# Kernel tuning notes

Hardware: AMD Instinct MI355X
Metric: run time of the kernel (lower is better)

## Reference

```python
import jax, jax.numpy as jnp
import numpy as np

D_MODEL = 1024
NUM_HEADS = 16
HEAD_DIM = D_MODEL // NUM_HEADS
THETA = 10000.0


def setup_inputs() -> dict:
    key = jax.random.key(0)
    k1, k2, k3 = jax.random.split(key, 3)
    B, S = 4, 2048
    std_qkv = (2.0 / (D_MODEL + 3 * D_MODEL)) ** 0.5
    std_out = (2.0 / (D_MODEL + D_MODEL)) ** 0.5
    return {
        "x": jax.random.normal(k1, (B, S, D_MODEL), dtype=jnp.float32),
        "token_positions": jnp.arange(S, dtype=jnp.int64 if jax.config.jax_enable_x64 else jnp.int32),
        "w_qkv": jax.random.normal(k2, (3 * D_MODEL, D_MODEL), dtype=jnp.float32) * std_qkv,
        "w_out": jax.random.normal(k3, (D_MODEL, D_MODEL), dtype=jnp.float32) * std_out,
    }


def _apply_rope(x, token_positions):
    # x: [b, h, s, d_h]; token_positions: [s]
    inv_freq = 1.0 / (THETA ** (jnp.arange(0, HEAD_DIM, 2, dtype=jnp.float32) / HEAD_DIM))
    angles = token_positions.astype(jnp.float32)[:, None] * inv_freq  # [s, d_h/2]
    cos, sin = jnp.cos(angles), jnp.sin(angles)
    x_even = x[..., 0::2]
    x_odd = x[..., 1::2]
    out_even = x_even * cos - x_odd * sin
    out_odd = x_even * sin + x_odd * cos
    # re-interleave even/odd lanes
    return jnp.stack([out_even, out_odd], axis=-1).reshape(x.shape)


def reference(x, token_positions, w_qkv, w_out):
    B, S, _ = x.shape
    qkv = jnp.einsum("bsd,ed->bse", x, w_qkv)  # [b, s, 3*d_model]
    q, k, v = jnp.split(qkv, 3, axis=-1)

    def to_heads(t):  # [b, s, d_model] -> [b, h, s, d_h]
        return t.reshape(B, S, NUM_HEADS, HEAD_DIM).transpose(0, 2, 1, 3)

    q, k, v = to_heads(q), to_heads(k), to_heads(v)
    q = _apply_rope(q, token_positions)
    k = _apply_rope(k, token_positions)

    scale = 1.0 / (HEAD_DIM ** 0.5)
    scores = jnp.einsum("bhqd,bhkd->bhqk", q, k) * scale  # [b, h, s, s]
    causal = jnp.tril(jnp.ones((S, S), dtype=bool))
    scores = jnp.where(causal, scores, -jnp.inf)
    probs = jax.nn.softmax(scores, axis=-1)
    out = jnp.einsum("bhqk,bhkd->bhqd", probs, v)  # [b, h, s, d_h]
    out = out.transpose(0, 2, 1, 3).reshape(B, S, D_MODEL)
    return jnp.einsum("bsd,ed->bse", out, w_out)
```

## Files before the change

### kernel.cpp

```cpp
#include <hip/hip_runtime.h>

typedef unsigned short u16;
typedef __attribute__((ext_vector_type(4))) float f32x4;
typedef __attribute__((ext_vector_type(8))) __bf16 bf16x8;
typedef __attribute__((ext_vector_type(8))) short short8;
typedef __attribute__((ext_vector_type(4))) u16 u16x4;

__device__ __forceinline__ u16 f2bf(float f) {
    union { float f; unsigned u; } v; v.f = f;
    unsigned r = v.u + 0x7fffu + ((v.u >> 16) & 1u);
    return (u16)(r >> 16);
}

__device__ __forceinline__ f32x4 mfma16(bf16x8 a, bf16x8 b, f32x4 c) {
    return __builtin_amdgcn_mfma_f32_16x16x32_bf16(a, b, c, 0, 0, 0);
}

__device__ __forceinline__ void gload16(const u16* g, u16* lds) {
    __builtin_amdgcn_global_load_lds(
        (const __attribute__((address_space(1))) void*)g,
        (__attribute__((address_space(3))) void*)lds, 16, 0, 0);
}

__global__ void cvt_bf16_kernel(const float* __restrict__ src, u16* __restrict__ dst, int n4) {
    int i = blockIdx.x * blockDim.x + threadIdx.x;
    if (i >= n4) return;
    float4 v = ((const float4*)src)[i];
    u16x4 o = { f2bf(v.x), f2bf(v.y), f2bf(v.z), f2bf(v.w) };
    *(u16x4*)&dst[i * 4] = o;
}

__global__ void rope_tbl_kernel(const int* __restrict__ pos, float2* __restrict__ tbl) {
    int i = blockIdx.x * blockDim.x + threadIdx.x;
    int s = i >> 5, p = i & 31;
    float inv = powf(10000.0f, -(float)p / 32.0f);
    float a = (float)pos[s] * inv;
    float sn, cs;
    sincosf(a, &sn, &cs);
    tbl[i] = make_float2(cs, sn);
}

template<int MODE>
__global__ __launch_bounds__(256) void gemm_bt(
    const u16* __restrict__ A, const u16* __restrict__ B,
    float* __restrict__ C, int N,
    u16* __restrict__ Qt, u16* __restrict__ Ktn, u16* __restrict__ VTt,
    const float2* __restrict__ tbl)
{
    __shared__ alignas(16) u16 As[128 * 32];
    __shared__ alignas(16) u16 Bs[128 * 32];
    const int t = threadIdx.x;
    const int l = t & 63, w = t >> 6;
    const int lg = l >> 4, lc = l & 15;
    const int wr = w >> 1, wc = w & 1;
    const int brow = blockIdx.y * 128, bcol = blockIdx.x * 128;
    const int sr = w * 16 + (l >> 2), sc = (l & 3) * 8;
    const u16* ga = A + (size_t)(brow + sr) * 1024 + sc;
    const u16* gb = B + (size_t)(bcol + sr) * 1024 + sc;
    u16* la = &As[w * 512];
    u16* lb = &Bs[w * 512];
    f32x4 acc[4][4] = {};

    for (int kt = 0; kt < 1024; kt += 32) {
        __syncthreads();
        gload16(ga + kt, la);
        gload16(ga + 64 * 1024 + kt, la + 2048);
        gload16(gb + kt, lb);
        gload16(gb + 64 * 1024 + kt, lb + 2048);
        __syncthreads();
        bf16x8 af[4], bfr[4];
#pragma unroll
        for (int i = 0; i < 4; ++i)
            af[i] = *(const bf16x8*)&As[(wr * 64 + i * 16 + lc) * 32 + lg * 8];
#pragma unroll
        for (int j = 0; j < 4; ++j)
            bfr[j] = *(const bf16x8*)&Bs[(wc * 64 + j * 16 + lc) * 32 + lg * 8];
#pragma unroll
        for (int i = 0; i < 4; ++i)
#pragma unroll
            for (int j = 0; j < 4; ++j)
                acc[i][j] = mfma16(af[i], bfr[j], acc[i][j]);
    }

    if (MODE == 0) {
#pragma unroll
        for (int i = 0; i < 4; ++i) {
            int row = brow + wr * 64 + i * 16 + lg * 4;
#pragma unroll
            for (int j = 0; j < 4; ++j) {
                int col = bcol + wc * 64 + j * 16 + lc;
#pragma unroll
                for (int jj = 0; jj < 4; ++jj)
                    C[(size_t)(row + jj) * N + col] = acc[i][j][jj];
            }
        }
    } else {
        const int b = brow >> 11;
#pragma unroll
        for (int i = 0; i < 4; ++i) {
            int s0 = (brow & 2047) + wr * 64 + i * 16 + lg * 4;
#pragma unroll
            for (int j = 0; j < 4; ++j) {
                int e0 = bcol + wc * 64 + j * 16;
                int region = e0 >> 10;
                int er = e0 & 1023;
                int h = er >> 6;
                int d = (er & 63) + lc;
                size_t bh = (size_t)(b * 16 + h);
                if (region <= 1) {
                    int p = d >> 1;
                    float sgn = (d & 1) ? 1.0f : -1.0f;
                    u16* dst = (region == 0) ? Qt : Ktn;
                    float mul = (region == 0) ? 0.18033688011112043f : 1.0f;
#pragma unroll
                    for (int jj = 0; jj < 4; ++jj) {
                        float v = acc[i][j][jj];
                        float pr = __shfl_xor(v, 1);
                        float2 cs = tbl[(size_t)(s0 + jj) * 32 + p];
                        float o = (v * cs.x + pr * cs.y * sgn) * mul;
                        int s = s0 + jj;
                        int dd = (region == 0) ? d : (d ^ ((s & 7) << 3));
                        dst[((size_t)bh * 2048 + s) * 64 + dd] = f2bf(o);
                    }
                } else {
                    int tile = s0 >> 6, r = s0 & 63;
                    int p0 = ((r >> 5) << 5) + (((r >> 2) & 3) << 3) + (((r >> 4) & 1) << 2);
                    int idx = (tile << 6) + (p0 ^ ((d & 7) << 3));
                    u16x4 pk;
#pragma unroll
                    for (int jj = 0; jj < 4; ++jj) pk[jj] = f2bf(acc[i][j][jj]);
                    *(u16x4*)&VTt[((size_t)bh * 64 + d) * 2048 + idx] = pk;
                }
            }
        }
    }
}

__global__ __launch_bounds__(256, 4) void attn_kernel(
    const u16* __restrict__ Qt, const u16* __restrict__ Kswz,
    const u16* __restrict__ Vp, u16* __restrict__ O)
{
    __shared__ alignas(16) u16 Kl[2][64 * 64];
    __shared__ alignas(16) u16 Vl[2][64 * 64];
    const int bid = blockIdx.x;
    const int qt = 15 - (bid >> 6);
    const int bh = bid & 63;
    const int t = threadIdx.x, l = t & 63, w = t >> 6;
    const int lg = l >> 4, lc = l & 15;
    const int qb0 = qt * 128 + w * 32;
    const int ntiles = 2 * qt + 2;
    const int swz = (lc & 7) << 3;

    bf16x8 qf[2][2];
#pragma unroll
    for (int f = 0; f < 2; ++f)
#pragma unroll
        for (int fk = 0; fk < 2; ++fk)
            qf[f][fk] = *(const bf16x8*)&Qt[((size_t)bh * 2048 + qb0 + 16 * f + lc) * 64 + fk * 32 + lg * 8];

    const bf16x8 ones = { (__bf16)1.f, (__bf16)1.f, (__bf16)1.f, (__bf16)1.f,
                          (__bf16)1.f, (__bf16)1.f, (__bf16)1.f, (__bf16)1.f };

    f32x4 aco[2][4] = {};
    f32x4 aco_sum[2] = {};
    float m[2] = { -1e30f, -1e30f };

    const int srow = t >> 3;
    const int scol = (t & 7) * 8;
    const u16* gK = Kswz + (size_t)bh * 131072;
    const u16* gV = Vp + (size_t)bh * 131072;

    auto stage = [&](int buf, int kv0) {
        gload16(gK + ((size_t)(kv0 + srow) << 6) + scol,      &Kl[buf][srow * 64 + scol]);
        gload16(gK + ((size_t)(kv0 + srow + 32) << 6) + scol, &Kl[buf][(srow + 32) * 64 + scol]);
        gload16(gV + (size_t)srow * 2048 + kv0 + scol,        &Vl[buf][srow * 64 + scol]);
        gload16(gV + (size_t)(srow + 32) * 2048 + kv0 + scol, &Vl[buf][(srow + 32) * 64 + scol]);
    };

    stage(0, 0);
    __syncthreads();
    int cur = 0;

    for (int kt = 0; kt < ntiles; ++kt) {
        const int kv0 = kt * 64;
        if (kt + 1 < ntiles) stage(cur ^ 1, kv0 + 64);

        if (kv0 <= qb0 + 31) {
            const u16* Kc = Kl[cur];
            const u16* Vc = Vl[cur];

            f32x4 sc[2][4];
            const f32x4 zf = { 0.f, 0.f, 0.f, 0.f };
#pragma unroll
            for (int nb = 0; nb < 4; ++nb) {
                const u16* kr = &Kc[(nb * 16 + lc) * 64];
                bf16x8 kb0 = *(const bf16x8*)&kr[(lg * 8) ^ swz];
                bf16x8 kb1 = *(const bf16x8*)&kr[(32 + lg * 8) ^ swz];
                sc[0][nb] = mfma16(kb0, qf[0][0], zf);
                sc[0][nb] = mfma16(kb1, qf[0][1], sc[0][nb]);
                sc[1][nb] = mfma16(kb0, qf[1][0], zf);
                sc[1][nb] = mfma16(kb1, qf[1][1], sc[1][nb]);
            }

            float pm[2];
#pragma unroll
            for (int f = 0; f < 2; ++f) {
                if (kv0 + 63 > qb0 + 16 * f) {
                    const int qq = qb0 + 16 * f + lc;
#pragma unroll
                    for (int nb = 0; nb < 4; ++nb) {
                        const int kb = kv0 + nb * 16 + lg * 4;
#pragma unroll
                        for (int jj = 0; jj < 4; ++jj)
                            if (kb + jj > qq) sc[f][nb][jj] = -1e38f;
                    }
                }
                float a0 = fmaxf(fmaxf(sc[f][0][0], sc[f][0][1]), fmaxf(sc[f][0][2], sc[f][0][3]));
                float a1 = fmaxf(fmaxf(sc[f][1][0], sc[f][1][1]), fmaxf(sc[f][1][2], sc[f][1][3]));
                float a2 = fmaxf(fmaxf(sc[f][2][0], sc[f][2][1]), fmaxf(sc[f][2][2], sc[f][2][3]));
                float a3 = fmaxf(fmaxf(sc[f][3][0], sc[f][3][1]), fmaxf(sc[f][3][2], sc[f][3][3]));
                float a = fmaxf(fmaxf(a0, a1), fmaxf(a2, a3));
                a = fmaxf(a, __shfl_xor(a, 16));
                a = fmaxf(a, __shfl_xor(a, 32));
                pm[f] = a;
            }

            int need = (pm[0] > m[0] + 11.0f) || (pm[1] > m[1] + 11.0f);
            if (__any(need)) {
#pragma unroll
                for (int f = 0; f < 2; ++f) {
                    float mn = fmaxf(m[f], pm[f]);
                    float scal = exp2f(m[f] - mn);
                    m[f] = mn;
                    aco_sum[f][0] *= scal;
#pragma unroll
                    for (int nb = 0; nb < 4; ++nb) aco[f][nb] *= scal;
                }
            }

            bf16x8 pB[2][2];
#pragma unroll
            for (int f = 0; f < 2; ++f) {
#pragma unroll
                for (int nb = 0; nb < 4; ++nb)
#pragma unroll
                    for (int jj = 0; jj < 4; ++jj)
                        sc[f][nb][jj] = exp2f(sc[f][nb][jj] - m[f]);
#pragma unroll
                for (int fk = 0; fk < 2; ++fk) {
                    bf16x8 pb;
#pragma unroll
                    for (int e = 0; e < 4; ++e) {
                        pb[e]     = (__bf16)sc[f][2 * fk][e];
                        pb[e + 4] = (__bf16)sc[f][2 * fk + 1][e];
                    }
                    pB[f][fk] = pb;
                }
            }

#pragma unroll
            for (int nb = 0; nb < 4; ++nb) {
                const u16* vr = &Vc[(nb * 16 + lc) * 64];
#pragma unroll
                for (int fk = 0; fk < 2; ++fk) {
                    bf16x8 va = *(const bf16x8*)&vr[(fk * 32 + lg * 8) ^ swz];
                    aco[0][nb] = mfma16(va, pB[0][fk], aco[0][nb]);
                    aco[1][nb] = mfma16(va, pB[1][fk], aco[1][nb]);
                }
            }
#pragma unroll
            for (int f = 0; f < 2; ++f) {
                aco_sum[f] = mfma16(ones, pB[f][0], aco_sum[f]);
                aco_sum[f] = mfma16(ones, pB[f][1], aco_sum[f]);
            }
        }

        __syncthreads();
        cur ^= 1;
    }

    const int b = bh >> 4, h = bh & 15;
#pragma unroll
    for (int f = 0; f < 2; ++f) {
        float rinv = 1.0f / aco_sum[f][0];
        size_t row = (size_t)b * 2048 + qb0 + 16 * f + lc;
#pragma unroll
        for (int nb = 0; nb < 4; ++nb) {
            u16x4 pk;
#pragma unroll
            for (int jj = 0; jj < 4; ++jj) pk[jj] = f2bf(aco[f][nb][jj] * rinv);
            *(u16x4*)&O[row * 1024 + h * 64 + nb * 16 + lg * 4] = pk;
        }
    }
}

extern "C" void kernel_launch(void* const* d_in, const int* in_sizes, int n_in,
                              void* d_out, int out_size, void* d_ws, size_t ws_size,
                              hipStream_t stream) {
    const float* x    = (const float*)d_in[0];
    const int*   pos  = (const int*)d_in[1];
    const float* wqkv = (const float*)d_in[2];
    const float* wout = (const float*)d_in[3];
    float* out = (float*)d_out;
    char* ws = (char*)d_ws;

    u16*    x_bf    = (u16*)(ws);
    u16*    wqkv_bf = (u16*)(ws + 16777216);
    u16*    wout_bf = (u16*)(ws + 23068672);
    float2* tbl     = (float2*)(ws + 25165824);
    u16*    Qt      = (u16*)(ws + 25690112);
    u16*    Kt      = (u16*)(ws + 42467328);
    u16*    VTt     = (u16*)(ws + 59244544);
    u16*    O       = (u16*)(ws + 76021760);
    if (ws_size < 92798976u) return;

    cvt_bf16_kernel<<<8192, 256, 0, stream>>>(x, x_bf, 2097152);
    cvt_bf16_kernel<<<3072, 256, 0, stream>>>(wqkv, wqkv_bf, 786432);
    cvt_bf16_kernel<<<1024, 256, 0, stream>>>(wout, wout_bf, 262144);
    rope_tbl_kernel<<<256, 256, 0, stream>>>(pos, tbl);

    dim3 g1(24, 64);
    gemm_bt<1><<<g1, 256, 0, stream>>>(x_bf, wqkv_bf, nullptr, 0, Qt, Kt, VTt, tbl);

    attn_kernel<<<1024, 256, 0, stream>>>(Qt, Kt, VTt, O);

    dim3 g2(8, 64);
    gemm_bt<0><<<g2, 256, 0, stream>>>(O, wout_bf, out, 1024, nullptr, nullptr, nullptr, nullptr);
}
```

Baseline: 310.0 us.

## Load V fragments directly from global in MFMA order, stage 128-row K tiles

The QKV projection now writes V in a fragment-major layout, so each lane's bf16x8 MFMA operand is contiguous. The attention kernel reads V straight from global/L2 into registers instead of staging it through LDS, and stages K in 128-row tiles processed as two 64-row subtiles, which halves the number of barriers per block. It also reorders query-tile scheduling to interleave heavy and light causal tiles, and raises wave priority around the MFMA sections. The aim is to cut LDS traffic and synchronisation cost. In exchange, V loads now expose global-memory latency inside the loop, and the larger K buffer uses the same total LDS.

```diff
diff --git a/kernel.cpp b/kernel.cpp
--- a/kernel.cpp
+++ b/kernel.cpp
@@ -124,12 +124,14 @@
                     }
                 } else {
                     int tile = s0 >> 6, r = s0 & 63;
-                    int p0 = ((r >> 5) << 5) + (((r >> 2) & 3) << 3) + (((r >> 4) & 1) << 2);
-                    int idx = (tile << 6) + (p0 ^ ((d & 7) << 3));
+                    int fk = r >> 5, lgg = (r >> 2) & 3, eb = ((r >> 4) & 1) * 4;
+                    size_t off = bh * 131072 + (size_t)tile * 4096 +
+                                 (size_t)(d >> 4) * 1024 + fk * 512 + lgg * 128 +
+                                 (d & 15) * 8 + eb;
                     u16x4 pk;
 #pragma unroll
                     for (int jj = 0; jj < 4; ++jj) pk[jj] = f2bf(acc[i][j][jj]);
-                    *(u16x4*)&VTt[((size_t)bh * 64 + d) * 2048 + idx] = pk;
+                    *(u16x4*)&VTt[off] = pk;
                 }
             }
         }
@@ -138,17 +140,20 @@
 
 __global__ __launch_bounds__(256, 4) void attn_kernel(
     const u16* __restrict__ Qt, const u16* __restrict__ Kswz,
-    const u16* __restrict__ Vp, u16* __restrict__ O)
+    const u16* __restrict__ Vg, u16* __restrict__ O)
 {
-    __shared__ alignas(16) u16 Kl[2][64 * 64];
-    __shared__ alignas(16) u16 Vl[2][64 * 64];
+    __shared__ alignas(16) u16 Kl[2][128 * 64];
     const int bid = blockIdx.x;
-    const int qt = 15 - (bid >> 6);
+    const int rr_ = bid >> 8, aa_ = (bid >> 6) & 3;
     const int bh = bid & 63;
+    const int qt = (rr_ == 0) ? 15 - 2 * aa_
+                 : (rr_ == 1) ? 8 + 2 * aa_
+                 : (rr_ == 2) ? 7 - 2 * aa_
+                              : 2 * aa_;
     const int t = threadIdx.x, l = t & 63, w = t >> 6;
     const int lg = l >> 4, lc = l & 15;
     const int qb0 = qt * 128 + w * 32;
-    const int ntiles = 2 * qt + 2;
+    const int ntiles = qt + 1;
     const int swz = (lc & 7) << 3;
 
     bf16x8 qf[2][2];
@@ -168,110 +173,122 @@
     const int srow = t >> 3;
     const int scol = (t & 7) * 8;
     const u16* gK = Kswz + (size_t)bh * 131072;
-    const u16* gV = Vp + (size_t)bh * 131072;
-
-    auto stage = [&](int buf, int kv0) {
-        gload16(gK + ((size_t)(kv0 + srow) << 6) + scol,      &Kl[buf][srow * 64 + scol]);
-        gload16(gK + ((size_t)(kv0 + srow + 32) << 6) + scol, &Kl[buf][(srow + 32) * 64 + scol]);
-        gload16(gV + (size_t)srow * 2048 + kv0 + scol,        &Vl[buf][srow * 64 + scol]);
-        gload16(gV + (size_t)(srow + 32) * 2048 + kv0 + scol, &Vl[buf][(srow + 32) * 64 + scol]);
+    const u16* gV = Vg + (size_t)bh * 131072 + l * 8;
+
+    auto stageK = [&](int buf, int kv0) {
+#pragma unroll
+        for (int c = 0; c < 4; ++c)
+            gload16(gK + ((size_t)(kv0 + srow + 32 * c) << 6) + scol,
+                    &Kl[buf][(srow + 32 * c) * 64 + scol]);
     };
 
-    stage(0, 0);
+    stageK(0, 0);
     __syncthreads();
     int cur = 0;
 
     for (int kt = 0; kt < ntiles; ++kt) {
-        const int kv0 = kt * 64;
-        if (kt + 1 < ntiles) stage(cur ^ 1, kv0 + 64);
-
-        if (kv0 <= qb0 + 31) {
-            const u16* Kc = Kl[cur];
-            const u16* Vc = Vl[cur];
-
-            f32x4 sc[2][4];
-            const f32x4 zf = { 0.f, 0.f, 0.f, 0.f };
-#pragma unroll
-            for (int nb = 0; nb < 4; ++nb) {
-                const u16* kr = &Kc[(nb * 16 + lc) * 64];
-                bf16x8 kb0 = *(const bf16x8*)&kr[(lg * 8) ^ swz];
-                bf16x8 kb1 = *(const bf16x8*)&kr[(32 + lg * 8) ^ swz];
-                sc[0][nb] = mfma16(kb0, qf[0][0], zf);
-                sc[0][nb] = mfma16(kb1, qf[0][1], sc[0][nb]);
-                sc[1][nb] = mfma16(kb0, qf[1][0], zf);
-                sc[1][nb] = mfma16(kb1, qf[1][1], sc[1][nb]);
-            }
-
-            float pm[2];
-#pragma unroll
-            for (int f = 0; f < 2; ++f) {
-                if (kv0 + 63 > qb0 + 16 * f) {
-                    const int qq = qb0 + 16 * f + lc;
-#pragma unroll
-                    for (int nb = 0; nb < 4; ++nb) {
-                        const int kb = kv0 + nb * 16 + lg * 4;
+        const int kv0 = kt * 128;
+        if (kt + 1 < ntiles) stageK(cur ^ 1, kv0 + 128);
+
+#pragma unroll
+        for (int sub = 0; sub < 2; ++sub) {
+            const int kvs = kv0 + sub * 64;
+            if (kvs <= qb0 + 31) {
+                const u16* Kc = &Kl[cur][(sub << 6) * 64];
+
+                f32x4 sc[2][4];
+                const f32x4 zf = { 0.f, 0.f, 0.f, 0.f };
+                __builtin_amdgcn_s_setprio(1);
+#pragma unroll
+                for (int nb = 0; nb < 4; ++nb) {
+                    const u16* kr = &Kc[(nb * 16 + lc) * 64];
+                    bf16x8 kb0 = *(const bf16x8*)&kr[(lg * 8) ^ swz];
+                    bf16x8 kb1 = *(const bf16x8*)&kr[(32 + lg * 8) ^ swz];
+                    sc[0][nb] = mfma16(kb0, qf[0][0], zf);
+                    sc[0][nb] = mfma16(kb1, qf[0][1], sc[0][nb]);
+                    sc[1][nb] = mfma16(kb0, qf[1][0], zf);
+                    sc[1][nb] = mfma16(kb1, qf[1][1], sc[1][nb]);
+                }
+                __builtin_amdgcn_s_setprio(0);
+
+                float pm[2];
+#pragma unroll
+                for (int f = 0; f < 2; ++f) {
+                    if (kvs + 63 > qb0 + 16 * f) {
+                        const int qq = qb0 + 16 * f + lc;
+#pragma unroll
+                        for (int nb = 0; nb < 4; ++nb) {
+                            const int kb = kvs + nb * 16 + lg * 4;
+#pragma unroll
+                            for (int jj = 0; jj < 4; ++jj)
+                                if (kb + jj > qq) sc[f][nb][jj] = -1e38f;
+                        }
+                    }
+                    float a0 = fmaxf(fmaxf(sc[f][0][0], sc[f][0][1]), fmaxf(sc[f][0][2], sc[f][0][3]));
+                    float a1 = fmaxf(fmaxf(sc[f][1][0], sc[f][1][1]), fmaxf(sc[f][1][2], sc[f][1][3]));
+                    float a2 = fmaxf(fmaxf(sc[f][2][0], sc[f][2][1]), fmaxf(sc[f][2][2], sc[f][2][3]));
+                    float a3 = fmaxf(fmaxf(sc[f][3][0], sc[f][3][1]), fmaxf(sc[f][3][2], sc[f][3][3]));
+                    float a = fmaxf(fmaxf(a0, a1), fmaxf(a2, a3));
+                    a = fmaxf(a, __shfl_xor(a, 16));
+                    a = fmaxf(a, __shfl_xor(a, 32));
+                    pm[f] = a;
+                }
+
+                int need = (pm[0] > m[0] + 11.0f) || (pm[1] > m[1] + 11.0f);
+                if (__any(need)) {
+#pragma unroll
+                    for (int f = 0; f < 2; ++f) {
+                        float mn = fmaxf(m[f], pm[f]);
+                        float scal = exp2f(m[f] - mn);
+                        m[f] = mn;
+                        aco_sum[f][0] *= scal;
+#pragma unroll
+                        for (int nb = 0; nb < 4; ++nb) aco[f][nb] *= scal;
+                    }
+                }
+
+                bf16x8 pB[2][2];
+#pragma unroll
+                for (int f = 0; f < 2; ++f) {
+#pragma unroll
+                    for (int nb = 0; nb < 4; ++nb)
 #pragma unroll
                         for (int jj = 0; jj < 4; ++jj)
-                            if (kb + jj > qq) sc[f][nb][jj] = -1e38f;
-                    }
-                }
-                float a0 = fmaxf(fmaxf(sc[f][0][0], sc[f][0][1]), fmaxf(sc[f][0][2], sc[f][0][3]));
-                float a1 = fmaxf(fmaxf(sc[f][1][0], sc[f][1][1]), fmaxf(sc[f][1][2], sc[f][1][3]));
-                float a2 = fmaxf(fmaxf(sc[f][2][0], sc[f][2][1]), fmaxf(sc[f][2][2], sc[f][2][3]));
-                float a3 = fmaxf(fmaxf(sc[f][3][0], sc[f][3][1]), fmaxf(sc[f][3][2], sc[f][3][3]));
-                float a = fmaxf(fmaxf(a0, a1), fmaxf(a2, a3));
-                a = fmaxf(a, __shfl_xor(a, 16));
-                a = fmaxf(a, __shfl_xor(a, 32));
-                pm[f] = a;
-            }
-
-            int need = (pm[0] > m[0] + 11.0f) || (pm[1] > m[1] + 11.0f);
-            if (__any(need)) {
+                            sc[f][nb][jj] = exp2f(sc[f][nb][jj] - m[f]);
+#pragma unroll
+                    for (int fk = 0; fk < 2; ++fk) {
+                        bf16x8 pb;
+#pragma unroll
+                        for (int e = 0; e < 4; ++e) {
+                            pb[e]     = (__bf16)sc[f][2 * fk][e];
+                            pb[e + 4] = (__bf16)sc[f][2 * fk + 1][e];
+                        }
+                        pB[f][fk] = pb;
+                    }
+                }
+
+                const u16* vt = gV + ((size_t)(2 * kt + sub) << 12);
+                bf16x8 va[4][2];
+#pragma unroll
+                for (int nb = 0; nb < 4; ++nb)
+#pragma unroll
+                    for (int fk = 0; fk < 2; ++fk)
+                        va[nb][fk] = *(const bf16x8*)(vt + nb * 1024 + fk * 512);
+
+                __builtin_amdgcn_s_setprio(1);
+#pragma unroll
+                for (int nb = 0; nb < 4; ++nb)
+#pragma unroll
+                    for (int fk = 0; fk < 2; ++fk) {
+                        aco[0][nb] = mfma16(va[nb][fk], pB[0][fk], aco[0][nb]);
+                        aco[1][nb] = mfma16(va[nb][fk], pB[1][fk], aco[1][nb]);
+                    }
 #pragma unroll
                 for (int f = 0; f < 2; ++f) {
-                    float mn = fmaxf(m[f], pm[f]);
-                    float scal = exp2f(m[f] - mn);
-                    m[f] = mn;
-                    aco_sum[f][0] *= scal;
-#pragma unroll
-                    for (int nb = 0; nb < 4; ++nb) aco[f][nb] *= scal;
-                }
-            }
-
-            bf16x8 pB[2][2];
-#pragma unroll
-            for (int f = 0; f < 2; ++f) {
-#pragma unroll
-                for (int nb = 0; nb < 4; ++nb)
-#pragma unroll
-                    for (int jj = 0; jj < 4; ++jj)
-                        sc[f][nb][jj] = exp2f(sc[f][nb][jj] - m[f]);
-#pragma unroll
-                for (int fk = 0; fk < 2; ++fk) {
-                    bf16x8 pb;
-#pragma unroll
-                    for (int e = 0; e < 4; ++e) {
-                        pb[e]     = (__bf16)sc[f][2 * fk][e];
-                        pb[e + 4] = (__bf16)sc[f][2 * fk + 1][e];
-                    }
-                    pB[f][fk] = pb;
-                }
-            }
-
-#pragma unroll
-            for (int nb = 0; nb < 4; ++nb) {
-                const u16* vr = &Vc[(nb * 16 + lc) * 64];
-#pragma unroll
-                for (int fk = 0; fk < 2; ++fk) {
-                    bf16x8 va = *(const bf16x8*)&vr[(fk * 32 + lg * 8) ^ swz];
-                    aco[0][nb] = mfma16(va, pB[0][fk], aco[0][nb]);
-                    aco[1][nb] = mfma16(va, pB[1][fk], aco[1][nb]);
-                }
-            }
-#pragma unroll
-            for (int f = 0; f < 2; ++f) {
-                aco_sum[f] = mfma16(ones, pB[f][0], aco_sum[f]);
-                aco_sum[f] = mfma16(ones, pB[f][1], aco_sum[f]);
+                    aco_sum[f] = mfma16(ones, pB[f][0], aco_sum[f]);
+                    aco_sum[f] = mfma16(ones, pB[f][1], aco_sum[f]);
+                }
+                __builtin_amdgcn_s_setprio(0);
             }
         }
 
```

New measurement: 293.7 us. 1.06x faster.
